# Optimization experiments

Measured on AMD Instinct MI355X. Metric: run time of the kernel, lower is better.

Reference implementation:

```python
import math
import jax, jax.numpy as jnp
import numpy as np

B, S, D, H = 2, 2048, 2048, 16
HD = D // H  # 128
EPS = 1e-5


def setup_inputs() -> dict:
    key = jax.random.key(0)
    ks = jax.random.split(key, 7)
    x = jax.random.normal(ks[0], (B, S, D), jnp.float32)
    # RoPE tables: (seqlen, head_dim//2)
    theta = 10000.0
    inv_freq = 1.0 / (theta ** (np.arange(0, HD, 2, dtype=np.float32) / HD))
    t = np.arange(S, dtype=np.float32)
    freqs = np.outer(t, inv_freq)  # (S, HD//2)
    freqs_cos = jnp.asarray(np.cos(freqs), jnp.float32)
    freqs_sin = jnp.asarray(np.sin(freqs), jnp.float32)
    sc = 0.02
    wq = jax.random.normal(ks[1], (D, D), jnp.float32) * sc  # stored (in, out)
    wk = jax.random.normal(ks[2], (D, D), jnp.float32) * sc
    wv = jax.random.normal(ks[3], (D, D), jnp.float32) * sc
    wu = jax.random.normal(ks[4], (D, D), jnp.float32) * sc
    wo = jax.random.normal(ks[5], (D, D), jnp.float32) * sc
    norm_w = jnp.ones((D,), jnp.float32)
    return {"x": x, "freqs_cos": freqs_cos, "freqs_sin": freqs_sin,
            "wq": wq, "wk": wk, "wv": wv, "wu": wu, "wo": wo, "norm_w": norm_w}


def _rope(t, cos, sin):
    # t: (B, S, H, HD); cos/sin: (S, HD//2)
    tr = t.reshape(t.shape[:-1] + (-1, 2))
    r, i = tr[..., 0], tr[..., 1]
    c = cos[None, :, None, :]
    s = sin[None, :, None, :]
    out_r = r * c - i * s
    out_i = r * s + i * c
    return jnp.stack([out_r, out_i], axis=-1).reshape(t.shape)


def reference(x, freqs_cos, freqs_sin, wq, wk, wv, wu, wo, norm_w):
    b, s, d = x.shape
    h = jax.nn.silu(x)  # pre-projection SiLU on the input
    q = (h @ wq).reshape(b, s, H, HD)
    k = (h @ wk).reshape(b, s, H, HD)
    v = (h @ wv).reshape(b, s, H, HD)
    u = h @ wu  # reshape->transpose->flatten in original is identity on (b,s,d)
    q = _rope(q, freqs_cos, freqs_sin)
    k = _rope(k, freqs_cos, freqs_sin)
    # scores: (b, H, s, s)
    scores = jnp.einsum('bqhd,bkhd->bhqk', q, k) / math.sqrt(HD)
    causal = jnp.tril(jnp.ones((s, s), bool))  # mask!=0 positions zeroed; silu(0)=0
    scores = jnp.where(causal[None, None], jax.nn.silu(scores), 0.0)
    out = jnp.einsum('bhqk,bkhd->bqhd', scores, v).reshape(b, s, d)
    # RMSNorm
    out = out * jax.lax.rsqrt(jnp.mean(out * out, axis=-1, keepdims=True) + EPS)
    out = out * norm_w
    out = out * u
    return out @ wo
```

## Files before the change

kernel.cpp:

```cpp
#include <hip/hip_runtime.h>
#include <hip/hip_bf16.h>
#include <cstdint>

typedef __attribute__((ext_vector_type(8))) short bf16x8;
typedef __attribute__((ext_vector_type(4))) float f32x4;
typedef unsigned short u16;

constexpr int B = 2, S = 2048, D = 2048, H = 16, HD = 128;
constexpr int M = B * S;
constexpr int NQKU = 6144;
constexpr float SCALE = 0.08838834764831845f;

static __device__ __forceinline__ float b2f(u16 u) {
    union { float f; uint32_t i; } v; v.i = ((uint32_t)u) << 16; return v.f;
}
static __device__ __forceinline__ u16 f2b(float f) {
    union { float f; uint32_t i; } v; v.f = f;
    uint32_t x = v.i;
    return (u16)((x + 0x7FFFu + ((x >> 16) & 1u)) >> 16);
}

__device__ __forceinline__ void gll16(const void* g, void* l) {
    __builtin_amdgcn_global_load_lds(
        (const __attribute__((address_space(1))) uint32_t*)g,
        (__attribute__((address_space(3))) uint32_t*)l, 16, 0, 0);
}

#define BAR() do { asm volatile("" ::: "memory"); __builtin_amdgcn_s_barrier(); \
                   asm volatile("" ::: "memory"); } while (0)

__global__ __launch_bounds__(256) void silu_cast(const float* __restrict__ x,
                                                 u16* __restrict__ h, int n) {
    int i = (blockIdx.x * 256 + threadIdx.x) * 4;
    if (i >= n) return;
    float4 v = *(const float4*)(x + i);
    ushort4 o;
    o.x = f2b(v.x / (1.f + __expf(-v.x)));
    o.y = f2b(v.y / (1.f + __expf(-v.y)));
    o.z = f2b(v.z / (1.f + __expf(-v.z)));
    o.w = f2b(v.w / (1.f + __expf(-v.w)));
    *(ushort4*)(h + i) = o;
}

__global__ __launch_bounds__(256)
void wcast5(const float* __restrict__ w0, const float* __restrict__ w1,
            const float* __restrict__ w2, const float* __restrict__ w3,
            const float* __restrict__ w4, u16* __restrict__ wT) {
    __shared__ float t[64][65];
    int z = blockIdx.z;
    const float* w = (z == 0) ? w0 : (z == 1) ? w1 : (z == 2) ? w2 : (z == 3) ? w3 : w4;
    u16* dst = wT + (size_t)z * D * D;
    int tx = threadIdx.x & 63, ty = threadIdx.x >> 6;
    int kb = blockIdx.y * 64, nb = blockIdx.x * 64;
    for (int r = ty; r < 64; r += 4)
        t[r][tx] = w[(size_t)(kb + r) * D + nb + tx];
    __syncthreads();
    for (int r = ty; r < 64; r += 4)
        dst[(size_t)(nb + r) * D + kb + tx] = f2b(t[tx][r]);
}

__global__ __launch_bounds__(512, 2)
void gemm_qkuv(const u16* __restrict__ A, const u16* __restrict__ BT,
               u16* __restrict__ qku, u16* __restrict__ vt,
               u16* __restrict__ qr, u16* __restrict__ kr,
               const float* __restrict__ fc, const float* __restrict__ fs) {
    __shared__ u16 lds[65536];
    const int tid = threadIdx.x;
    const int lane = tid & 63, wid = tid >> 6;
    const int wm = wid >> 2, wn = wid & 3;
    const int l16 = lane & 15, lq = lane >> 4;

    const int orig = blockIdx.x;
    const int swz = (orig & 7) * 64 + (orig >> 3);
    const int mt = swz & 15, nt = swz >> 4;
    const int m0 = mt * 256, n0 = nt * 256;

    const int srow = tid >> 2;
    const int ce = ((tid & 3) * 8) ^ (((tid >> 5) & 1) << 4);
    const int rdx = (lq * 16) ^ (((l16 >> 3) & 1) << 5);

    const u16* As0 = A + (size_t)(m0 + srow) * D + ce;
    const u16* Bs0 = BT + (size_t)(n0 + srow) * D + ce;

    {
        u16* dA = lds + wid * 512;
        u16* dB = lds + 16384 + wid * 512;
        gll16(As0,                    dA);
        gll16(As0 + (size_t)128 * D,  dA + 8192);
        gll16(Bs0,                    dB);
        gll16(Bs0 + (size_t)128 * D,  dB + 8192);
        gll16(As0 + 32,                    dA + 4096);
        gll16(As0 + 32 + (size_t)128 * D,  dA + 8192 + 4096);
        gll16(Bs0 + 32,                    dB + 4096);
        gll16(Bs0 + 32 + (size_t)128 * D,  dB + 8192 + 4096);
        u16* dA1 = lds + 32768 + wid * 512;
        u16* dB1 = lds + 32768 + 16384 + wid * 512;
        gll16(As0 + 64,                    dA1);
        gll16(As0 + 64 + (size_t)128 * D,  dA1 + 8192);
        gll16(Bs0 + 64,                    dB1);
        gll16(Bs0 + 64 + (size_t)128 * D,  dB1 + 8192);
    }
    asm volatile("s_waitcnt vmcnt(8)" ::: "memory");
    BAR();

    f32x4 acc[8][4] = {};
    bf16x8 a[8];
    const int rbB = (wn & 1) * 4096;

#define LOAD_A(kk)                                                            \
    _Pragma("unroll") for (int mi = 0; mi < 8; ++mi)                          \
        a[mi] = *(const bf16x8*)(Abase + (kk) * 8192 +                        \
                                 (mi * 16 + l16) * 64 + rdx);
#define LOAD_B(dst, nia, kk)                                                  \
    dst = *(const bf16x8*)(Bbase + (kk) * 8192 + rbB +                        \
                           ((nia) * 16 + l16) * 64 + rdx);
#define MFMA2(n0i, n1i)                                                       \
    __builtin_amdgcn_s_setprio(1);                                            \
    _Pragma("unroll") for (int mi = 0; mi < 8; ++mi) {                        \
        acc[mi][n0i] = __builtin_amdgcn_mfma_f32_16x16x32_bf16(a[mi], b0,     \
                            acc[mi][n0i], 0, 0, 0);                           \
        acc[mi][n1i] = __builtin_amdgcn_mfma_f32_16x16x32_bf16(a[mi], b1,     \
                            acc[mi][n1i], 0, 0, 0);                           \
    }                                                                          \
    __builtin_amdgcn_s_setprio(0);

    for (int kt = 0; kt < 32; ++kt) {
        const int buf = kt & 1;
        const char* Abase = (const char*)lds + buf * 65536 + wm * 16384;
        const char* Bbase = (const char*)lds + 32768 + buf * 65536 + (wn >> 1) * 16384;
        const bool st1 = (kt + 1) < 32;
        const bool st2 = (kt + 2) < 32;
        const u16* Asrc1 = As0 + (kt + 1) * 64;
        const u16* Bsrc1 = Bs0 + (kt + 1) * 64;
        const u16* Asrc2 = As0 + (kt + 2) * 64;
        const u16* Bsrc2 = Bs0 + (kt + 2) * 64;
        u16* dN = lds + (buf ^ 1) * 32768 + wid * 512;
        u16* dC = lds + buf * 32768 + wid * 512;
        bf16x8 b0, b1;

        LOAD_A(0);
        LOAD_B(b0, 0, 0);
        LOAD_B(b1, 1, 0);
        if (st1) { gll16(Asrc1 + 32, dN + 4096);
                   gll16(Asrc1 + 32 + (size_t)128 * D, dN + 8192 + 4096); }
        BAR();
        MFMA2(0, 1);
        BAR();
        LOAD_B(b0, 2, 0);
        LOAD_B(b1, 3, 0);
        if (st1) { gll16(Bsrc1 + 32, dN + 16384 + 4096);
                   gll16(Bsrc1 + 32 + (size_t)128 * D, dN + 16384 + 8192 + 4096); }
        BAR();
        MFMA2(2, 3);
        if (kt == 31) asm volatile("s_waitcnt vmcnt(0)" ::: "memory");
        else          asm volatile("s_waitcnt vmcnt(8)" ::: "memory");
        BAR();
        LOAD_A(1);
        LOAD_B(b0, 0, 1);
        LOAD_B(b1, 1, 1);
        if (st2) { gll16(Asrc2, dC);
                   gll16(Asrc2 + (size_t)128 * D, dC + 8192); }
        BAR();
        MFMA2(0, 1);
        BAR();
        LOAD_B(b0, 2, 1);
        LOAD_B(b1, 3, 1);
        if (st2) { gll16(Bsrc2, dC + 16384);
                   gll16(Bsrc2 + (size_t)128 * D, dC + 16384 + 8192); }
        BAR();
        MFMA2(2, 3);
        if (kt < 30)       asm volatile("s_waitcnt vmcnt(8)" ::: "memory");
        else if (kt == 30) asm volatile("s_waitcnt vmcnt(4)" ::: "memory");
        BAR();
    }
#undef LOAD_A
#undef LOAD_B
#undef MFMA2

    if (n0 >= NQKU) {
#pragma unroll
        for (int mi = 0; mi < 8; ++mi)
#pragma unroll
            for (int ni = 0; ni < 4; ++ni) {
                int c = n0 - NQKU + wn * 64 + ni * 16 + l16;
                int hh = c >> 7, d = c & 127;
                int row0 = m0 + wm * 128 + mi * 16 + lq * 4;
                int bb = row0 >> 11, s0 = row0 & 2047;
                ushort4 pk = make_ushort4(f2b(acc[mi][ni][0]), f2b(acc[mi][ni][1]),
                                          f2b(acc[mi][ni][2]), f2b(acc[mi][ni][3]));
                *(ushort4*)(vt + (((size_t)(bb * H + hh) * HD + d) * S + s0)) = pk;
            }
    } else if (n0 >= 4096) {
#pragma unroll
        for (int mi = 0; mi < 8; ++mi)
#pragma unroll
            for (int ni = 0; ni < 4; ++ni)
#pragma unroll
                for (int r = 0; r < 4; ++r) {
                    int row = m0 + wm * 128 + mi * 16 + lq * 4 + r;
                    int col = n0 + wn * 64 + ni * 16 + l16;
                    qku[(size_t)row * NQKU + col] = f2b(acc[mi][ni][r]);
                }
    } else {
        u16* dst = (n0 < 2048) ? qr : kr;
#pragma unroll
        for (int mi = 0; mi < 8; ++mi)
#pragma unroll
            for (int ni = 0; ni < 4; ++ni) {
                int c = (n0 & 2047) + wn * 64 + ni * 16 + l16;
                int hh = c >> 7, d = c & 127;
                int pp = d >> 1;
                float sgn = (d & 1) ? 1.f : -1.f;
                int row0 = m0 + wm * 128 + mi * 16 + lq * 4;
                int bb = row0 >> 11, s0 = row0 & 2047;
                u16* dp = dst + ((size_t)(bb * H + hh) * S + s0) * HD + d;
#pragma unroll
                for (int r = 0; r < 4; ++r) {
                    float me = acc[mi][ni][r];
                    float pt = __shfl_xor(me, 1, 64);
                    int sgl = s0 + r;
                    float cs = fc[sgl * 64 + pp], sn = fs[sgl * 64 + pp];
                    dp[(size_t)r * HD] = f2b(me * cs + sgn * pt * sn);
                }
            }
    }
}

__global__ __launch_bounds__(256)
void gemm_bt_f32(const u16* __restrict__ A, const u16* __restrict__ BT,
                 float* __restrict__ out, int lda, int ldc, int Kk) {
    __shared__ u16 As[128 * 32];
    __shared__ u16 Bs[128 * 32];
    const int tid = threadIdx.x;
    const int lane = tid & 63, w = tid >> 6;
    const int wm = w >> 1, wn = w & 1;
    const int l16 = lane & 15, lq = lane >> 4;
    const int m0 = blockIdx.y * 128, n0 = blockIdx.x * 128;
    const int rs = lane >> 2;
    const int cs = (lane & 3) * 8;
    f32x4 acc[4][4] = {};

    const u16* Ab = A + (size_t)(m0 + w * 32 + rs) * lda + cs;
    const u16* Bb = BT + (size_t)(n0 + w * 32 + rs) * Kk + cs;
    u16* Al = As + w * 32 * 32;
    u16* Bl = Bs + w * 32 * 32;

    for (int k0 = 0; k0 < Kk; k0 += 32) {
        gll16(Ab + k0, Al);
        gll16(Ab + k0 + (size_t)16 * lda, Al + 16 * 32);
        gll16(Bb + k0, Bl);
        gll16(Bb + k0 + (size_t)16 * Kk, Bl + 16 * 32);
        __syncthreads();
        bf16x8 af[4], bfr[4];
#pragma unroll
        for (int mi = 0; mi < 4; mi++)
            af[mi] = *(const bf16x8*)(As + (wm * 64 + mi * 16 + l16) * 32 + lq * 8);
#pragma unroll
        for (int ni = 0; ni < 4; ni++)
            bfr[ni] = *(const bf16x8*)(Bs + (wn * 64 + ni * 16 + l16) * 32 + lq * 8);
#pragma unroll
        for (int mi = 0; mi < 4; mi++)
#pragma unroll
            for (int ni = 0; ni < 4; ni++)
                acc[mi][ni] = __builtin_amdgcn_mfma_f32_16x16x32_bf16(
                    af[mi], bfr[ni], acc[mi][ni], 0, 0, 0);
        __syncthreads();
    }
#pragma unroll
    for (int mi = 0; mi < 4; mi++)
#pragma unroll
        for (int ni = 0; ni < 4; ni++)
#pragma unroll
            for (int r = 0; r < 4; r++) {
                int row = m0 + wm * 64 + mi * 16 + lq * 4 + r;
                int col = n0 + wn * 64 + ni * 16 + l16;
                out[(size_t)row * ldc + col] = acc[mi][ni][r];
            }
}

__global__ __launch_bounds__(512, 1)
void hstu_attn(const u16* __restrict__ qr, const u16* __restrict__ kr,
               const u16* __restrict__ vt, u16* __restrict__ attb) {
    __shared__ u16 k_l[2 * 8192];
    __shared__ u16 v_l[2 * 8192];
    __shared__ u16 s_l[128 * 72];
    const int id = blockIdx.x;
    const int bh = (id & 7) * 4 + ((id >> 3) & 3);
    const int slot = id >> 5;
    const int b = bh >> 4, h = bh & 15;
    const int tid = threadIdx.x, lane = tid & 63, w = tid >> 6;
    const int l16 = lane & 15, lq = lane >> 4;
    const int wq = w >> 2, wk4 = w & 3;

    const u16* kb = kr + (size_t)bh * S * HD;
    const u16* vb = vt + (size_t)bh * HD * S;
    const u16* qb = qr + (size_t)bh * S * HD;

#define STAGE_K(k0_, bf_) do {                                                \
    _Pragma("unroll") for (int r_ = 0; r_ < 2; ++r_) {                        \
        int i_ = tid + r_ * 512;                                              \
        int row_ = i_ >> 4, iu_ = i_ & 15;                                    \
        int uc_ = iu_ ^ (row_ & 7);                                           \
        gll16(kb + (size_t)((k0_) + row_) * HD + uc_ * 8,                     \
              k_l + (bf_) * 8192 + ((w * 64 + r_ * 512) << 3));               \
    } } while (0)
#define STAGE_V(k0_, bf_) do {                                                \
    _Pragma("unroll") for (int r_ = 0; r_ < 2; ++r_) {                        \
        int i_ = tid + r_ * 512;                                              \
        int d_ = i_ >> 3, iu_ = i_ & 7;                                       \
        int uc_ = iu_ ^ (d_ & 7);                                             \
        gll16(vb + (size_t)d_ * S + (k0_) + uc_ * 8,                          \
              v_l + (bf_) * 8192 + ((w * 64 + r_ * 512) << 3));               \
    } } while (0)

    for (int pass = 0; pass < 2; ++pass) {
        const int tq = pass ? (15 - slot) : slot;
        const int q0 = tq * 128;
        const int kmax = 2 * tq + 1;

        bf16x8 qf[4][4];
#pragma unroll
        for (int mi = 0; mi < 4; ++mi)
#pragma unroll
            for (int kk = 0; kk < 4; ++kk)
                qf[mi][kk] = *(const bf16x8*)(qb +
                    (size_t)(q0 + wq * 64 + mi * 16 + l16) * HD + kk * 32 + lq * 8);
        f32x4 acco[4][2] = {};

        STAGE_K(0, 0);
        STAGE_V(0, 0);
        STAGE_K(64, 1);
        STAGE_V(64, 1);
        asm volatile("s_waitcnt vmcnt(8)" ::: "memory");
        BAR();

        for (int kt = 0; kt <= kmax; ++kt) {
            const int k0 = kt * 64;
            const int buf = kt & 1;
            f32x4 accs[4] = {};
            __builtin_amdgcn_s_setprio(1);
#pragma unroll
            for (int kk = 0; kk < 4; ++kk) {
                int row = wk4 * 16 + l16;
                bf16x8 kf = *(const bf16x8*)(k_l + buf * 8192 + row * 128 +
                            ((kk * 32 + lq * 8) ^ ((row & 7) << 3)));
#pragma unroll
                for (int mi = 0; mi < 4; ++mi)
                    accs[mi] = __builtin_amdgcn_mfma_f32_16x16x32_bf16(
                        qf[mi][kk], kf, accs[mi], 0, 0, 0);
            }
            __builtin_amdgcn_s_setprio(0);
            const bool dg = (kt >= 2 * tq);
#pragma unroll
            for (int mi = 0; mi < 4; ++mi)
#pragma unroll
                for (int r = 0; r < 4; ++r) {
                    int qrow = wq * 64 + mi * 16 + lq * 4 + r;
                    int krow = wk4 * 16 + l16;
                    float vv = accs[mi][r] * SCALE;
                    vv = (!dg || (k0 + krow <= q0 + qrow))
                             ? vv * __builtin_amdgcn_rcpf(1.f + __expf(-vv))
                             : 0.f;
                    s_l[qrow * 72 + krow] = f2b(vv);
                }
            BAR();
            if (kt + 2 <= kmax) STAGE_K((kt + 2) * 64, buf);
            if (kt <= kmax - 2)
                asm volatile("s_waitcnt vmcnt(12)" ::: "memory");
            else if (kt == kmax - 1)
                asm volatile("s_waitcnt vmcnt(8)" ::: "memory");
            else
                asm volatile("s_waitcnt vmcnt(0)" ::: "memory");
            BAR();
            __builtin_amdgcn_s_setprio(1);
#pragma unroll
            for (int kk = 0; kk < 2; ++kk) {
                bf16x8 sf[4];
#pragma unroll
                for (int mi = 0; mi < 4; ++mi)
                    sf[mi] = *(const bf16x8*)(s_l + (wq * 64 + mi * 16 + l16) * 72 +
                                              kk * 32 + lq * 8);
#pragma unroll
                for (int ni = 0; ni < 2; ++ni) {
                    int row = wk4 * 32 + ni * 16 + l16;
                    bf16x8 vf = *(const bf16x8*)(v_l + buf * 8192 + row * 64 +
                                (((kk * 4 + lq) ^ (row & 7)) << 3));
#pragma unroll
                    for (int mi = 0; mi < 4; ++mi)
                        acco[mi][ni] = __builtin_amdgcn_mfma_f32_16x16x32_bf16(
                            sf[mi], vf, acco[mi][ni], 0, 0, 0);
                }
            }
            __builtin_amdgcn_s_setprio(0);
            BAR();
            if (kt + 2 <= kmax) STAGE_V((kt + 2) * 64, buf);
            if (kt <= kmax - 2)
                asm volatile("s_waitcnt vmcnt(12)" ::: "memory");
            else if (kt == kmax - 1)
                asm volatile("s_waitcnt vmcnt(4)" ::: "memory");
            BAR();
        }
#pragma unroll
        for (int mi = 0; mi < 4; ++mi)
#pragma unroll
            for (int ni = 0; ni < 2; ++ni)
#pragma unroll
                for (int r = 0; r < 4; ++r)
                    attb[(size_t)(b * S + q0 + wq * 64 + mi * 16 + lq * 4 + r) * NQKU +
                         h * HD + wk4 * 32 + ni * 16 + l16] = f2b(acco[mi][ni][r]);
    }
#undef STAGE_K
#undef STAGE_V
}

__global__ __launch_bounds__(256)
void rms_mul(u16* __restrict__ qku, const float* __restrict__ nw) {
    int row = blockIdx.x;
    int tid = threadIdx.x;
    int col = tid * 8;
    u16 at[8];
    *(int4*)at = *(const int4*)(qku + (size_t)row * NQKU + col);
    float f[8];
    float ss = 0.f;
#pragma unroll
    for (int j = 0; j < 8; j++) { f[j] = b2f(at[j]); ss += f[j] * f[j]; }
#pragma unroll
    for (int off = 32; off > 0; off >>= 1) ss += __shfl_down(ss, off, 64);
    __shared__ float red[4];
    int lane = tid & 63, w = tid >> 6;
    if (lane == 0) red[w] = ss;
    __syncthreads();
    float rs = rsqrtf((red[0] + red[1] + red[2] + red[3]) * (1.f / D) + 1e-5f);
    u16* up = qku + (size_t)row * NQKU + 4096 + col;
    u16 ut[8];
    *(int4*)ut = *(const int4*)up;
    u16 o[8];
#pragma unroll
    for (int j = 0; j < 8; j++)
        o[j] = f2b(f[j] * rs * nw[col + j] * b2f(ut[j]));
    *(int4*)up = *(int4*)o;
}

extern "C" void kernel_launch(void* const* d_in, const int* in_sizes, int n_in,
                              void* d_out, int out_size, void* d_ws, size_t ws_size,
                              hipStream_t stream) {
    const float* x  = (const float*)d_in[0];
    const float* fc = (const float*)d_in[1];
    const float* fs = (const float*)d_in[2];
    const float* wq = (const float*)d_in[3];
    const float* wk = (const float*)d_in[4];
    const float* wv = (const float*)d_in[5];
    const float* wu = (const float*)d_in[6];
    const float* wo = (const float*)d_in[7];
    const float* nw = (const float*)d_in[8];
    float* out = (float*)d_out;

    char* ws = (char*)d_ws;
    const size_t WSZ = (size_t)D * D * sizeof(u16);
    u16* h_b  = (u16*)(ws);
    u16* wT   = (u16*)(ws + 2 * WSZ);
    u16* qku  = (u16*)(ws + 7 * WSZ);
    u16* vt   = (u16*)(ws + 13 * WSZ);
    u16* k_r  = (u16*)(ws + 15 * WSZ);
    u16* q_r  = (u16*)(ws + 17 * WSZ);

    silu_cast<<<M * D / 1024, 256, 0, stream>>>(x, h_b, M * D);
    wcast5<<<dim3(32, 32, 5), 256, 0, stream>>>(wq, wk, wu, wv, wo, wT);

    gemm_qkuv<<<512, 512, 0, stream>>>(h_b, wT, qku, vt, q_r, k_r, fc, fs);

    hstu_attn<<<256, 512, 0, stream>>>(q_r, k_r, vt, qku);
    rms_mul<<<M, 256, 0, stream>>>(qku, nw);
    gemm_bt_f32<<<dim3(D / 128, M / 128), 256, 0, stream>>>(
        qku + 4096, wT + 4 * (size_t)D * D, out, NQKU, D, D);
}
```

Baseline: 317.1 us.

## Enlarge attention query tile to 256 rows and halve the grid

The HSTU attention kernel now processes 256 query rows per pass instead of 128, with waves rearranged as 4 query groups by 2 key groups. Each wave computes a 64x32 score tile and a 64x64 output tile, and the grid drops from 256 to 128 blocks. The goal is to reuse each staged K/V tile across twice as many query rows, cutting global K/V traffic and barriers per unit of work. The cost is half as many blocks, which leaves many compute units idle on a large GPU. It also raises register use for the accumulators, along with the matching retuning of the vmcnt waits.

Result: slower. 364.6 us (+15.0%).

```diff
diff --git a/kernel.cpp b/kernel.cpp
--- a/kernel.cpp
+++ b/kernel.cpp
@@ -283,14 +283,14 @@
                const u16* __restrict__ vt, u16* __restrict__ attb) {
     __shared__ u16 k_l[2 * 8192];
     __shared__ u16 v_l[2 * 8192];
-    __shared__ u16 s_l[128 * 72];
+    __shared__ u16 s_l[256 * 72];
     const int id = blockIdx.x;
     const int bh = (id & 7) * 4 + ((id >> 3) & 3);
     const int slot = id >> 5;
     const int b = bh >> 4, h = bh & 15;
     const int tid = threadIdx.x, lane = tid & 63, w = tid >> 6;
     const int l16 = lane & 15, lq = lane >> 4;
-    const int wq = w >> 2, wk4 = w & 3;
+    const int wq = w >> 1, wk2 = w & 1;
 
     const u16* kb = kr + (size_t)bh * S * HD;
     const u16* vb = vt + (size_t)bh * HD * S;
@@ -314,9 +314,9 @@
     } } while (0)
 
     for (int pass = 0; pass < 2; ++pass) {
-        const int tq = pass ? (15 - slot) : slot;
-        const int q0 = tq * 128;
-        const int kmax = 2 * tq + 1;
+        const int tq = pass ? (7 - slot) : slot;
+        const int q0 = tq * 256;
+        const int kmax = 4 * tq + 3;
 
         bf16x8 qf[4][4];
 #pragma unroll
@@ -325,50 +325,54 @@
             for (int kk = 0; kk < 4; ++kk)
                 qf[mi][kk] = *(const bf16x8*)(qb +
                     (size_t)(q0 + wq * 64 + mi * 16 + l16) * HD + kk * 32 + lq * 8);
-        f32x4 acco[4][2] = {};
+        f32x4 acco[4][4] = {};
 
         STAGE_K(0, 0);
         STAGE_V(0, 0);
         STAGE_K(64, 1);
         STAGE_V(64, 1);
-        asm volatile("s_waitcnt vmcnt(8)" ::: "memory");
+        asm volatile("s_waitcnt vmcnt(4)" ::: "memory");
         BAR();
 
         for (int kt = 0; kt <= kmax; ++kt) {
             const int k0 = kt * 64;
             const int buf = kt & 1;
-            f32x4 accs[4] = {};
+            f32x4 accs[4][2] = {};
             __builtin_amdgcn_s_setprio(1);
 #pragma unroll
-            for (int kk = 0; kk < 4; ++kk) {
-                int row = wk4 * 16 + l16;
-                bf16x8 kf = *(const bf16x8*)(k_l + buf * 8192 + row * 128 +
-                            ((kk * 32 + lq * 8) ^ ((row & 7) << 3)));
-#pragma unroll
-                for (int mi = 0; mi < 4; ++mi)
-                    accs[mi] = __builtin_amdgcn_mfma_f32_16x16x32_bf16(
-                        qf[mi][kk], kf, accs[mi], 0, 0, 0);
-            }
+            for (int kk = 0; kk < 4; ++kk)
+#pragma unroll
+                for (int ni = 0; ni < 2; ++ni) {
+                    int row = wk2 * 32 + ni * 16 + l16;
+                    bf16x8 kf = *(const bf16x8*)(k_l + buf * 8192 + row * 128 +
+                                ((kk * 32 + lq * 8) ^ ((row & 7) << 3)));
+#pragma unroll
+                    for (int mi = 0; mi < 4; ++mi)
+                        accs[mi][ni] = __builtin_amdgcn_mfma_f32_16x16x32_bf16(
+                            qf[mi][kk], kf, accs[mi][ni], 0, 0, 0);
+                }
             __builtin_amdgcn_s_setprio(0);
-            const bool dg = (kt >= 2 * tq);
+            const bool dg = (kt >= 4 * tq);
 #pragma unroll
             for (int mi = 0; mi < 4; ++mi)
 #pragma unroll
-                for (int r = 0; r < 4; ++r) {
-                    int qrow = wq * 64 + mi * 16 + lq * 4 + r;
-                    int krow = wk4 * 16 + l16;
-                    float vv = accs[mi][r] * SCALE;
-                    vv = (!dg || (k0 + krow <= q0 + qrow))
-                             ? vv * __builtin_amdgcn_rcpf(1.f + __expf(-vv))
-                             : 0.f;
-                    s_l[qrow * 72 + krow] = f2b(vv);
-                }
+                for (int ni = 0; ni < 2; ++ni)
+#pragma unroll
+                    for (int r = 0; r < 4; ++r) {
+                        int qrow = wq * 64 + mi * 16 + lq * 4 + r;
+                        int krow = wk2 * 32 + ni * 16 + l16;
+                        float vv = accs[mi][ni][r] * SCALE;
+                        vv = (!dg || (k0 + krow <= q0 + qrow))
+                                 ? vv * __builtin_amdgcn_rcpf(1.f + __expf(-vv))
+                                 : 0.f;
+                        s_l[qrow * 72 + krow] = f2b(vv);
+                    }
             BAR();
             if (kt + 2 <= kmax) STAGE_K((kt + 2) * 64, buf);
-            if (kt <= kmax - 2)
-                asm volatile("s_waitcnt vmcnt(12)" ::: "memory");
+            if (kt + 2 <= kmax)
+                asm volatile("s_waitcnt vmcnt(6)" ::: "memory");
             else if (kt == kmax - 1)
-                asm volatile("s_waitcnt vmcnt(8)" ::: "memory");
+                asm volatile("s_waitcnt vmcnt(4)" ::: "memory");
             else
                 asm volatile("s_waitcnt vmcnt(0)" ::: "memory");
             BAR();
@@ -381,8 +385,8 @@
                     sf[mi] = *(const bf16x8*)(s_l + (wq * 64 + mi * 16 + l16) * 72 +
                                               kk * 32 + lq * 8);
 #pragma unroll
-                for (int ni = 0; ni < 2; ++ni) {
-                    int row = wk4 * 32 + ni * 16 + l16;
+                for (int ni = 0; ni < 4; ++ni) {
+                    int row = wk2 * 64 + ni * 16 + l16;
                     bf16x8 vf = *(const bf16x8*)(v_l + buf * 8192 + row * 64 +
                                 (((kk * 4 + lq) ^ (row & 7)) << 3));
 #pragma unroll
@@ -393,21 +397,22 @@
             }
             __builtin_amdgcn_s_setprio(0);
             BAR();
-            if (kt + 2 <= kmax) STAGE_V((kt + 2) * 64, buf);
-            if (kt <= kmax - 2)
-                asm volatile("s_waitcnt vmcnt(12)" ::: "memory");
-            else if (kt == kmax - 1)
-                asm volatile("s_waitcnt vmcnt(4)" ::: "memory");
+            if (kt + 2 <= kmax) {
+                STAGE_V((kt + 2) * 64, buf);
+                asm volatile("s_waitcnt vmcnt(6)" ::: "memory");
+            } else if (kt == kmax - 1) {
+                asm volatile("s_waitcnt vmcnt(2)" ::: "memory");
+            }
             BAR();
         }
 #pragma unroll
         for (int mi = 0; mi < 4; ++mi)
 #pragma unroll
-            for (int ni = 0; ni < 2; ++ni)
+            for (int ni = 0; ni < 4; ++ni)
 #pragma unroll
                 for (int r = 0; r < 4; ++r)
                     attb[(size_t)(b * S + q0 + wq * 64 + mi * 16 + lq * 4 + r) * NQKU +
-                         h * HD + wk4 * 32 + ni * 16 + l16] = f2b(acco[mi][ni][r]);
+                         h * HD + wk2 * 64 + ni * 16 + l16] = f2b(acco[mi][ni][r]);
     }
 #undef STAGE_K
 #undef STAGE_V
@@ -469,7 +474,7 @@
 
     gemm_qkuv<<<512, 512, 0, stream>>>(h_b, wT, qku, vt, q_r, k_r, fc, fs);
 
-    hstu_attn<<<256, 512, 0, stream>>>(q_r, k_r, vt, qku);
+    hstu_attn<<<128, 512, 0, stream>>>(q_r, k_r, vt, qku);
     rms_mul<<<M, 256, 0, stream>>>(qku, nw);
     gemm_bt_f32<<<dim3(D / 128, M / 128), 256, 0, stream>>>(
         qku + 4096, wT + 4 * (size_t)D * D, out, NQKU, D, D);
```
